# Kernel tuning notes

Measured on AMD Instinct MI355X. Metric: run time of the kernel, lower is better.

The kernel has to match this reference:

```python
import jax, jax.numpy as jnp
import numpy as np

NEG_SLOPE = 0.2


def _gat_layer(x, src, dst, W, att_src, att_dst, bias, concat):
    # x: [N, Fin], W: [Fin, H*C], att_*: [H, C], bias: [H*C] or [C]
    N = x.shape[0]
    H, C = att_src.shape
    h = (x @ W).reshape(N, H, C)                      # node features per head
    a_src = jnp.sum(h * att_src, axis=-1)             # [N, H]
    a_dst = jnp.sum(h * att_dst, axis=-1)             # [N, H]
    e = jax.nn.leaky_relu(a_src[src] + a_dst[dst], NEG_SLOPE)  # [E, H]
    # segment softmax over destination nodes
    m = jax.ops.segment_max(e, dst, num_segments=N)   # [N, H]
    m = jnp.where(jnp.isfinite(m), m, 0.0)
    ex = jnp.exp(e - m[dst])
    s = jax.ops.segment_sum(ex, dst, num_segments=N)  # [N, H]
    alpha = ex / (s[dst] + 1e-16)                     # [E, H]
    msg = h[src] * alpha[:, :, None]                  # [E, H, C]
    out = jax.ops.segment_sum(msg, dst, num_segments=N)  # [N, H, C]
    out = out.reshape(N, H * C) if concat else out.mean(axis=1)
    return out + bias


def setup_inputs() -> dict:
    key = jax.random.key(0)
    ks = jax.random.split(key, 20)
    N, E, Fin, Cg, H = 50000, 800000, 128, 64, 4
    HC = H * Cg
    s = 0.1
    x = jax.random.normal(ks[0], (N, Fin), jnp.float32)
    edge_index = jax.random.randint(ks[1], (2, E), 0, N, dtype=jnp.int32)
    inp = {
        'x': x,
        'edge_index': edge_index,
        'W0': jax.random.normal(ks[2], (Fin, HC), jnp.float32) * s,
        'as0': jax.random.normal(ks[3], (H, Cg), jnp.float32) * s,
        'ad0': jax.random.normal(ks[4], (H, Cg), jnp.float32) * s,
        'b0': jnp.zeros((HC,), jnp.float32),
        'W1': jax.random.normal(ks[5], (HC, HC), jnp.float32) * s,
        'as1': jax.random.normal(ks[6], (H, Cg), jnp.float32) * s,
        'ad1': jax.random.normal(ks[7], (H, Cg), jnp.float32) * s,
        'b1': jnp.zeros((HC,), jnp.float32),
        'W2': jax.random.normal(ks[8], (HC, HC), jnp.float32) * s,
        'as2': jax.random.normal(ks[9], (H, Cg), jnp.float32) * s,
        'ad2': jax.random.normal(ks[10], (H, Cg), jnp.float32) * s,
        'b2': jnp.zeros((Cg,), jnp.float32),
        # linear head: 64 -> 128 -> 10
        'lw0': jax.random.normal(ks[11], (Cg, 128), jnp.float32) * s,
        'lb0': jnp.zeros((128,), jnp.float32),
        'lw1': jax.random.normal(ks[12], (128, 10), jnp.float32) * s,
        'lb1': jnp.zeros((10,), jnp.float32),
    }
    return inp


def reference(x, edge_index, W0, as0, ad0, b0, W1, as1, ad1, b1,
              W2, as2, ad2, b2, lw0, lb0, lw1, lb1):
    N = x.shape[0]
    # PyG GATConv add_self_loops=True: append self-loop edges
    loop = jnp.arange(N, dtype=edge_index.dtype)
    src = jnp.concatenate([edge_index[0], loop])
    dst = jnp.concatenate([edge_index[1], loop])
    h = _gat_layer(x, src, dst, W0, as0, ad0, b0, True)
    h = _gat_layer(h, src, dst, W1, as1, ad1, b1, True)
    h = _gat_layer(h, src, dst, W2, as2, ad2, b2, False)
    h = jax.nn.relu(h @ lw0 + lb0)
    return h @ lw1 + lb1
```

## Files before the change

### kernel.cpp

```cpp
#include <hip/hip_runtime.h>
#include <hip/hip_bf16.h>

#define HEADS 4
#define CH 64
#define HC 256

typedef __attribute__((ext_vector_type(8))) short short8;
typedef __attribute__((ext_vector_type(4))) float f32x4;
typedef __attribute__((ext_vector_type(8))) _Float16 half8;

typedef __attribute__((address_space(1))) const unsigned int as1_uint;
typedef __attribute__((address_space(3))) unsigned int as3_uint;

__device__ __forceinline__ void gll16(const void* g, void* l){
  __builtin_amdgcn_global_load_lds((as1_uint*)g, (as3_uint*)l, 16, 0, 0);
}

__device__ inline unsigned short f2bf(float f){
  unsigned u = __float_as_uint(f);
  return (unsigned short)((u + 0x7FFF + ((u >> 16) & 1)) >> 16);
}


__global__ void hist_kernel(const int* __restrict__ dst, int E, int ET, int* __restrict__ cnt){
  int e = blockIdx.x * blockDim.x + threadIdx.x;
  if (e >= ET) return;
  int d = (e < E) ? dst[e] : (e - E);
  atomicAdd(&cnt[d], 1);
}

__global__ void blocksum_kernel(const int* __restrict__ cnt, int N, int* __restrict__ bsum){
  int tid = threadIdx.x;
  int i = blockIdx.x * 256 + tid;
  int v = (i < N) ? cnt[i] : 0;
  #pragma unroll
  for (int off = 32; off >= 1; off >>= 1) v += __shfl_xor(v, off);
  __shared__ int ws[4];
  if ((tid & 63) == 0) ws[tid >> 6] = v;
  __syncthreads();
  if (tid == 0) bsum[blockIdx.x] = ws[0] + ws[1] + ws[2] + ws[3];
}

__global__ void scanb_kernel(int* __restrict__ bsum, int nb){
  __shared__ int buf[256];
  int tid = threadIdx.x;
  int v = (tid < nb) ? bsum[tid] : 0;
  buf[tid] = v;
  __syncthreads();
  #pragma unroll
  for (int off = 1; off < 256; off <<= 1){
    int t = (tid >= off) ? buf[tid - off] : 0;
    __syncthreads();
    buf[tid] += t;
    __syncthreads();
  }
  if (tid < nb) bsum[tid] = buf[tid] - v;
}

__global__ void scanfinal_kernel(const int* __restrict__ cnt, const int* __restrict__ bsum,
                                 int* __restrict__ ptr, int* __restrict__ cur, int N){
  __shared__ int buf[256];
  int tid = threadIdx.x;
  int i = blockIdx.x * 256 + tid;
  int v = (i < N) ? cnt[i] : 0;
  buf[tid] = v;
  __syncthreads();
  #pragma unroll
  for (int off = 1; off < 256; off <<= 1){
    int t = (tid >= off) ? buf[tid - off] : 0;
    __syncthreads();
    buf[tid] += t;
    __syncthreads();
  }
  int exc = buf[tid] - v + bsum[blockIdx.x];
  if (i < N){
    ptr[i] = exc; cur[i] = exc;
    if (i == N - 1) ptr[N] = exc + v;
  }
}

__global__ void scatter_kernel(const int* __restrict__ src, const int* __restrict__ dst,
                               int E, int ET, int* __restrict__ cur,
                               int* __restrict__ csr_src, int* __restrict__ csr_dst){
  int e = blockIdx.x * blockDim.x + threadIdx.x;
  if (e >= ET) return;
  int s, d;
  if (e < E){ s = src[e]; d = dst[e]; } else { s = e - E; d = e - E; }
  int pos = atomicAdd(&cur[d], 1);
  csr_src[pos] = s;
  csr_dst[pos] = d;
}


__global__ void dhist_kernel(const int* __restrict__ cnt, int N, int* __restrict__ dbins){
  __shared__ int lb[64];
  int tid = threadIdx.x;
  if (tid < 64) lb[tid] = 0;
  __syncthreads();
  int n = blockIdx.x * 256 + tid;
  if (n < N) atomicAdd(&lb[min(cnt[n], 63)], 1);
  __syncthreads();
  if (tid < 64 && lb[tid]) atomicAdd(&dbins[tid], lb[tid]);
}

__global__ void dscan_kernel(int* __restrict__ dbins, int* __restrict__ dcur){
  int lane = threadIdx.x;
  int v = dbins[lane];
  int s = v;
  #pragma unroll
  for (int off = 1; off < 64; off <<= 1){
    int t = __shfl_up(s, off);
    if (lane >= off) s += t;
  }
  int exc = s - v;
  dbins[lane] = exc;
  dcur[lane] = exc;
}

__global__ void dscatter_kernel(const int* __restrict__ cnt, int N, int* __restrict__ dcur,
                                int* __restrict__ perm){
  __shared__ int lb[64];
  __shared__ int base[64];
  int tid = threadIdx.x;
  if (tid < 64) lb[tid] = 0;
  __syncthreads();
  int n = blockIdx.x * 256 + tid;
  bool valid = n < N;
  int bin = 0, rank = 0;
  if (valid){
    bin = min(cnt[n], 63);
    rank = atomicAdd(&lb[bin], 1);
  }
  __syncthreads();
  if (tid < 64) base[tid] = lb[tid] ? atomicAdd(&dcur[tid], lb[tid]) : 0;
  __syncthreads();
  if (valid) perm[base[bin] + rank] = n;
}


__global__ void ew_kernel(const int* __restrict__ csr_src, const int* __restrict__ csr_dst,
                          const float* __restrict__ a_src, const float* __restrict__ a_dst,
                          float* __restrict__ w, int ET){
  int i = blockIdx.x * 256 + threadIdx.x;
  if (i >= ET) return;
  int s = csr_src[i], d = csr_dst[i];
  float4 as = *(const float4*)&a_src[(size_t)s * 4];
  float4 ad = *(const float4*)&a_dst[(size_t)d * 4];
  float4 r;
  float e;
  e = as.x + ad.x; e = e > 0.f ? e : 0.2f * e; r.x = __expf(e);
  e = as.y + ad.y; e = e > 0.f ? e : 0.2f * e; r.y = __expf(e);
  e = as.z + ad.z; e = e > 0.f ? e : 0.2f * e; r.z = __expf(e);
  e = as.w + ad.w; e = e > 0.f ? e : 0.2f * e; r.w = __expf(e);
  *(float4*)&w[(size_t)i * 4] = r;
}


__global__ void wsplit_kernel(const float* __restrict__ W0, unsigned short* __restrict__ h0,
                              unsigned short* __restrict__ l0,
                              const float* __restrict__ W1, unsigned short* __restrict__ h1,
                              unsigned short* __restrict__ l1,
                              const float* __restrict__ W2, unsigned short* __restrict__ h2,
                              unsigned short* __restrict__ l2){
  int idx = blockIdx.x * 256 + threadIdx.x;
  const float* W; unsigned short *hi, *lo; int K;
  if (idx < 128 * HC){ W = W0; hi = h0; lo = l0; K = 128; }
  else if (idx < (128 + 256) * HC){ idx -= 128 * HC; W = W1; hi = h1; lo = l1; K = 256; }
  else { idx -= (128 + 256) * HC; W = W2; hi = h2; lo = l2; K = 256; }
  int k = idx >> 8, n = idx & 255;
  float w = W[idx];
  unsigned short hb = f2bf(w);
  float hf = __uint_as_float((unsigned)hb << 16);
  unsigned short lb = f2bf(w - hf);
  hi[(size_t)n * K + k] = hb;
  lo[(size_t)n * K + k] = lb;
}


__global__ void xsplit_kernel(const float* __restrict__ x, int total4,
                              unsigned short* __restrict__ xhi, unsigned short* __restrict__ xlo){
  int i4 = blockIdx.x * 256 + threadIdx.x;
  if (i4 >= total4) return;
  float4 v = *(const float4*)&x[(size_t)i4 * 4];
  float va[4] = {v.x, v.y, v.z, v.w};
  unsigned short h4[4], l4[4];
  #pragma unroll
  for (int j = 0; j < 4; j++){
    unsigned short hb = f2bf(va[j]);
    float hf = __uint_as_float((unsigned)hb << 16);
    h4[j] = hb;
    l4[j] = f2bf(va[j] - hf);
  }
  *(ushort4*)&xhi[(size_t)i4 * 4] = make_ushort4(h4[0], h4[1], h4[2], h4[3]);
  *(ushort4*)&xlo[(size_t)i4 * 4] = make_ushort4(l4[0], l4[1], l4[2], l4[3]);
}


__global__ void lwsplit_kernel(const float* __restrict__ lw0,
                               unsigned short* __restrict__ l0hi, unsigned short* __restrict__ l0lo,
                               const float* __restrict__ lw1, _Float16* __restrict__ l1T){
  int idx = blockIdx.x * 256 + threadIdx.x;
  if (idx < 8192){
    int n = idx & 127, k = idx >> 7;
    float w = lw0[k * 128 + n];
    unsigned short hb = f2bf(w);
    float hf = __uint_as_float((unsigned)hb << 16);
    unsigned short lb = f2bf(w - hf);
    l0hi[n * 64 + k] = hb;
    l0lo[n * 64 + k] = lb;
  } else if (idx < 8192 + 2048){
    int id = idx - 8192;
    int n = id & 15, k = id >> 4;
    float w = (n < 10) ? lw1[k * 10 + n] : 0.f;
    l1T[n * 128 + k] = (_Float16)w;
  }
}


__launch_bounds__(256, 2)
__global__ void gemm_mfma_kernel(const unsigned short* __restrict__ Ahi,
                                 const unsigned short* __restrict__ Alo,
                                 const unsigned short* __restrict__ BhiT,
                                 const unsigned short* __restrict__ BloT,
                                 _Float16* __restrict__ Cm,
                                 const float* __restrict__ att_s, const float* __restrict__ att_d,
                                 float* __restrict__ a_src, float* __restrict__ a_dst,
                                 int K){
  __shared__ __align__(16) unsigned short L[2][4][4096];

  int tid = threadIdx.x;
  int m0 = blockIdx.x * 128, n0 = blockIdx.y * 128;
  int wave = tid >> 6, lane = tid & 63;
  int wm = (wave >> 1) * 64, wn = (wave & 1) * 64;
  int col = lane & 15, quad = lane >> 4;

  f32x4 acc[4][4];
  #pragma unroll
  for (int a = 0; a < 4; a++)
    #pragma unroll
    for (int b = 0; b < 4; b++)
      acc[a][b] = (f32x4){0.f, 0.f, 0.f, 0.f};

  const int nIter = K >> 5;

  auto stage = [&](int buf, int kk){
    #pragma unroll
    for (int i = 0; i < 2; i++){
      int slotbase = (wave * 2 + i) * 64;
      int slot = slotbase + lane;
      int m = slot >> 2;
      int q = (lane & 3) ^ ((m >> 1) & 3);
      size_t ga = (size_t)(m0 + m) * K + kk + q * 8;
      size_t gb = (size_t)(n0 + m) * K + kk + q * 8;
      int lo = slotbase * 8;
      gll16(&Ahi[ga],  &L[buf][0][lo]);
      gll16(&Alo[ga],  &L[buf][1][lo]);
      gll16(&BhiT[gb], &L[buf][2][lo]);
      gll16(&BloT[gb], &L[buf][3][lo]);
    }
  };

  stage(0, 0);

  for (int it = 0; it < nIter; it++){
    int buf = it & 1;
    __syncthreads();
    if (it + 1 < nIter) stage(buf ^ 1, (it + 1) << 5);

    short8 af[4][2], bf[4][2];
    #pragma unroll
    for (int t = 0; t < 4; t++){
      int rmA = wm + t * 16 + col;
      int rmB = wn + t * 16 + col;
      int sA = rmA * 4 + (quad ^ ((rmA >> 1) & 3));
      int sB = rmB * 4 + (quad ^ ((rmB >> 1) & 3));
      af[t][0] = *(const short8*)&L[buf][0][sA * 8];
      af[t][1] = *(const short8*)&L[buf][1][sA * 8];
      bf[t][0] = *(const short8*)&L[buf][2][sB * 8];
      bf[t][1] = *(const short8*)&L[buf][3][sB * 8];
    }
    #pragma unroll
    for (int mt = 0; mt < 4; mt++)
      #pragma unroll
      for (int nt = 0; nt < 4; nt++){
        acc[mt][nt] = __builtin_amdgcn_mfma_f32_16x16x32_bf16(af[mt][0], bf[nt][0], acc[mt][nt], 0, 0, 0);
        acc[mt][nt] = __builtin_amdgcn_mfma_f32_16x16x32_bf16(af[mt][1], bf[nt][0], acc[mt][nt], 0, 0, 0);
        acc[mt][nt] = __builtin_amdgcn_mfma_f32_16x16x32_bf16(af[mt][0], bf[nt][1], acc[mt][nt], 0, 0, 0);
      }
  }

  #pragma unroll
  for (int mt = 0; mt < 4; mt++)
    #pragma unroll
    for (int nt = 0; nt < 4; nt++){
      int colg = n0 + wn + nt * 16 + col;
      #pragma unroll
      for (int r = 0; r < 4; r++){
        int row = m0 + wm + mt * 16 + quad * 4 + r;
        Cm[(size_t)row * HC + colg] = (_Float16)acc[mt][nt][r];
      }
    }

  int head = (n0 + wn) >> 6;
  float asv[4], adv[4];
  #pragma unroll
  for (int nt = 0; nt < 4; nt++){
    asv[nt] = att_s[head * CH + nt * 16 + col];
    adv[nt] = att_d[head * CH + nt * 16 + col];
  }
  #pragma unroll
  for (int mt = 0; mt < 4; mt++){
    float sp[4] = {0.f,0.f,0.f,0.f}, dp[4] = {0.f,0.f,0.f,0.f};
    #pragma unroll
    for (int nt = 0; nt < 4; nt++)
      #pragma unroll
      for (int r = 0; r < 4; r++){
        sp[r] += acc[mt][nt][r] * asv[nt];
        dp[r] += acc[mt][nt][r] * adv[nt];
      }
    #pragma unroll
    for (int off = 1; off <= 8; off <<= 1)
      #pragma unroll
      for (int r = 0; r < 4; r++){
        sp[r] += __shfl_xor(sp[r], off);
        dp[r] += __shfl_xor(dp[r], off);
      }
    if (col == 0){
      #pragma unroll
      for (int r = 0; r < 4; r++){
        int row = m0 + wm + mt * 16 + quad * 4 + r;
        a_src[row * HEADS + head] = sp[r];
        a_dst[row * HEADS + head] = dp[r];
      }
    }
  }
}


__global__ void agg_kernel(const _Float16* __restrict__ h, const float* __restrict__ w,
                           const int* __restrict__ ptr, const int* __restrict__ csr_src,
                           const int* __restrict__ perm,
                           const float* __restrict__ bias,
                           unsigned short* __restrict__ out_hi, unsigned short* __restrict__ out_lo,
                           int mean_mode, const float* __restrict__ b2,
                           float* __restrict__ f2){
  __shared__ float sm[HEADS][8][CH];
  int head = threadIdx.x >> 6;
  int lane = threadIdx.x & 63;
  int slot = lane >> 3, c8 = lane & 7;
  int pn = perm[blockIdx.x * 8 + slot];
  int beg = 0, deg = 0;
  if (pn >= 0){ beg = ptr[pn]; deg = ptr[pn + 1] - beg; }

  int maxdeg = deg;
  #pragma unroll
  for (int off = 8; off <= 32; off <<= 1) maxdeg = max(maxdeg, __shfl_xor(maxdeg, off));

  float acc[8] = {0.f,0.f,0.f,0.f,0.f,0.f,0.f,0.f};
  float ss = 0.f;
  int it = 0;
  for (; it + 4 <= maxdeg; it += 4){
    int idx[4]; float wv[4];
    #pragma unroll
    for (int k = 0; k < 4; k++)
      idx[k] = beg + ((it + k < deg) ? it + k : 0);
    int s0 = csr_src[idx[0]], s1 = csr_src[idx[1]];
    int s2 = csr_src[idx[2]], s3 = csr_src[idx[3]];
    #pragma unroll
    for (int k = 0; k < 4; k++)
      wv[k] = (it + k < deg) ? w[(size_t)idx[k] * 4 + head] : 0.f;
    half8 h0 = *(const half8*)&h[(size_t)s0 * HC + head * CH + c8 * 8];
    half8 h1 = *(const half8*)&h[(size_t)s1 * HC + head * CH + c8 * 8];
    half8 h2 = *(const half8*)&h[(size_t)s2 * HC + head * CH + c8 * 8];
    half8 h3 = *(const half8*)&h[(size_t)s3 * HC + head * CH + c8 * 8];
    #pragma unroll
    for (int j = 0; j < 8; j++){
      acc[j] += wv[0] * (float)h0[j];
      acc[j] += wv[1] * (float)h1[j];
      acc[j] += wv[2] * (float)h2[j];
      acc[j] += wv[3] * (float)h3[j];
    }
    ss += wv[0] + wv[1] + wv[2] + wv[3];
  }
  for (; it < maxdeg; ++it){
    bool valid = it < deg;
    int idx = beg + (valid ? it : 0);
    int s = csr_src[idx];
    float wv = valid ? w[(size_t)idx * 4 + head] : 0.f;
    half8 hv = *(const half8*)&h[(size_t)s * HC + head * CH + c8 * 8];
    #pragma unroll
    for (int j = 0; j < 8; j++) acc[j] += wv * (float)hv[j];
    ss += wv;
  }
  float inv = 1.f / (ss + 1e-16f);
  #pragma unroll
  for (int j = 0; j < 8; j++) acc[j] *= inv;

  if (!mean_mode){
    if (pn >= 0){
      const float* bp = &bias[head * CH + c8 * 8];
      short8 hi8, lo8;
      #pragma unroll
      for (int j = 0; j < 8; j++){
        float v = acc[j] + bp[j];
        unsigned short hb = f2bf(v);
        float hf = __uint_as_float((unsigned)hb << 16);
        hi8[j] = (short)hb;
        lo8[j] = (short)f2bf(v - hf);
      }
      size_t o = (size_t)pn * HC + head * CH + c8 * 8;
      *(short8*)&out_hi[o] = hi8;
      *(short8*)&out_lo[o] = lo8;
    }
  } else {
    #pragma unroll
    for (int j = 0; j < 8; j++) sm[head][slot][c8 * 8 + j] = acc[j];
    __syncthreads();
    for (int t = threadIdx.x; t < 512; t += 256){
      int sl = t >> 6, ch = t & 63;
      int pn2 = perm[blockIdx.x * 8 + sl];
      if (pn2 >= 0)
        f2[(size_t)pn2 * CH + ch] =
          0.25f * (sm[0][sl][ch] + sm[1][sl][ch] + sm[2][sl][ch] + sm[3][sl][ch]) + b2[ch];
    }
  }
}


__launch_bounds__(256, 2)
__global__ void head_mfma_kernel(const float* __restrict__ f2,
                                 const unsigned short* __restrict__ lw0hiT,
                                 const unsigned short* __restrict__ lw0loT,
                                 const _Float16* __restrict__ lw1T,
                                 const float* __restrict__ lb0,
                                 const float* __restrict__ lb1,
                                 float* __restrict__ outp, int N){
  __shared__ __align__(16) unsigned short L[27648];
  __shared__ __align__(16) _Float16 Ls[16][136];
  const int tid = threadIdx.x;
  const int wave = tid >> 6, lane = tid & 63;
  const int col = lane & 15, quad = lane >> 4;
  const int m0 = blockIdx.x * 64;

  { int n = tid >> 4, k = (tid & 15) * 8;
    *(half8*)&Ls[n][k] = *(const half8*)&lw1T[n * 128 + k]; }

  #pragma unroll
  for (int r = 0; r < 2; r++){
    int id = r * 256 + tid;
    int m = id >> 3, q = id & 7;
    int gm = m0 + m;
    float va[8];
    if (gm < N){
      float4 v0 = *(const float4*)&f2[(size_t)gm * CH + q * 8];
      float4 v1 = *(const float4*)&f2[(size_t)gm * CH + q * 8 + 4];
      va[0]=v0.x; va[1]=v0.y; va[2]=v0.z; va[3]=v0.w;
      va[4]=v1.x; va[5]=v1.y; va[6]=v1.z; va[7]=v1.w;
    } else {
      #pragma unroll
      for (int j = 0; j < 8; j++) va[j] = 0.f;
    }
    short8 hi8, lo8;
    #pragma unroll
    for (int j = 0; j < 8; j++){
      unsigned short hb = f2bf(va[j]);
      float hf = __uint_as_float((unsigned)hb << 16);
      hi8[j] = (short)hb;
      lo8[j] = (short)f2bf(va[j] - hf);
    }
    *(short8*)&L[m * 72 + q * 8] = hi8;
    *(short8*)&L[4608 + m * 72 + q * 8] = lo8;
  }
  #pragma unroll
  for (int r = 0; r < 4; r++){
    int id = r * 256 + tid;
    int n = id >> 3, q = id & 7;
    *(short8*)&L[9216 + n * 72 + q * 8]  = *(const short8*)&lw0hiT[n * 64 + q * 8];
    *(short8*)&L[18432 + n * 72 + q * 8] = *(const short8*)&lw0loT[n * 64 + q * 8];
  }
  __syncthreads();

  const int wn = wave * 32;
  f32x4 acc[4][2];
  #pragma unroll
  for (int a = 0; a < 4; a++)
    #pragma unroll
    for (int b = 0; b < 2; b++) acc[a][b] = (f32x4){0.f,0.f,0.f,0.f};

  #pragma unroll
  for (int ks = 0; ks < 2; ks++){
    int k = ks * 32 + quad * 8;
    short8 ah[4], al[4], bh[2], bl[2];
    #pragma unroll
    for (int mt = 0; mt < 4; mt++){
      ah[mt] = *(short8*)&L[(mt * 16 + col) * 72 + k];
      al[mt] = *(short8*)&L[4608 + (mt * 16 + col) * 72 + k];
    }
    #pragma unroll
    for (int nt = 0; nt < 2; nt++){
      bh[nt] = *(short8*)&L[9216 + (wn + nt * 16 + col) * 72 + k];
      bl[nt] = *(short8*)&L[18432 + (wn + nt * 16 + col) * 72 + k];
    }
    #pragma unroll
    for (int mt = 0; mt < 4; mt++)
      #pragma unroll
      for (int nt = 0; nt < 2; nt++){
        acc[mt][nt] = __builtin_amdgcn_mfma_f32_16x16x32_bf16(ah[mt], bh[nt], acc[mt][nt], 0, 0, 0);
        acc[mt][nt] = __builtin_amdgcn_mfma_f32_16x16x32_bf16(al[mt], bh[nt], acc[mt][nt], 0, 0, 0);
        acc[mt][nt] = __builtin_amdgcn_mfma_f32_16x16x32_bf16(ah[mt], bl[nt], acc[mt][nt], 0, 0, 0);
      }
  }
  __syncthreads();

  _Float16* Zp = (_Float16*)L;
  #pragma unroll
  for (int nt = 0; nt < 2; nt++){
    int n = wn + nt * 16 + col;
    float b = lb0[n];
    #pragma unroll
    for (int mt = 0; mt < 4; mt++)
      #pragma unroll
      for (int r2 = 0; r2 < 4; r2++){
        int m = mt * 16 + quad * 4 + r2;
        float z = acc[mt][nt][r2] + b;
        Zp[m * 136 + n] = (_Float16)fmaxf(z, 0.f);
      }
  }
  __syncthreads();

  f32x4 acc2 = (f32x4){0.f,0.f,0.f,0.f};
  #pragma unroll
  for (int ks = 0; ks < 4; ks++){
    int k = ks * 32 + quad * 8;
    half8 a2 = *(half8*)&Zp[(wave * 16 + col) * 136 + k];
    half8 b2v = *(half8*)&Ls[col][k];
    acc2 = __builtin_amdgcn_mfma_f32_16x16x32_f16(a2, b2v, acc2, 0, 0, 0);
  }
  if (col < 10){
    float bb = lb1[col];
    #pragma unroll
    for (int r2 = 0; r2 < 4; r2++){
      int row = m0 + wave * 16 + quad * 4 + r2;
      if (row < N) outp[(size_t)row * 10 + col] = acc2[r2] + bb;
    }
  }
}


extern "C" void kernel_launch(void* const* d_in, const int* in_sizes, int n_in,
                              void* d_out, int out_size, void* d_ws, size_t ws_size,
                              hipStream_t stream) {
  const float* x   = (const float*)d_in[0];
  const int*   ei  = (const int*)d_in[1];
  const float* W0  = (const float*)d_in[2];
  const float* as0 = (const float*)d_in[3];
  const float* ad0 = (const float*)d_in[4];
  const float* b0  = (const float*)d_in[5];
  const float* W1  = (const float*)d_in[6];
  const float* as1 = (const float*)d_in[7];
  const float* ad1 = (const float*)d_in[8];
  const float* b1  = (const float*)d_in[9];
  const float* W2  = (const float*)d_in[10];
  const float* as2 = (const float*)d_in[11];
  const float* ad2 = (const float*)d_in[12];
  const float* b2  = (const float*)d_in[13];
  const float* lw0 = (const float*)d_in[14];
  const float* lb0 = (const float*)d_in[15];
  const float* lw1 = (const float*)d_in[16];
  const float* lb1 = (const float*)d_in[17];
  float* outp = (float*)d_out;

  int N  = in_sizes[0] / 128;
  int E  = in_sizes[1] / 2;
  int ET = E + N;
  int nb = (N + 255) / 256;
  int Mp = ((N + 127) / 128) * 128;
  int Np8 = ((N + 7) / 8) * 8;

  char* ws = (char*)d_ws;
  _Float16* Hb = (_Float16*)ws;       ws += (size_t)Mp * HC * sizeof(_Float16);
  unsigned short* Fhi = (unsigned short*)ws; ws += (size_t)Mp * HC * 2;
  unsigned short* Flo = (unsigned short*)ws; ws += (size_t)Mp * HC * 2;
  float* f2  = (float*)ws; ws += (size_t)N * CH * sizeof(float);
  float* a_s = (float*)ws; ws += (size_t)Mp * HEADS * sizeof(float);
  float* a_d = (float*)ws; ws += (size_t)Mp * HEADS * sizeof(float);
  float* ewt = (float*)ws; ws += (size_t)ET * HEADS * sizeof(float);
  int* cnt   = (int*)ws;   ws += (size_t)N * sizeof(int);
  int* cur   = (int*)ws;   ws += (size_t)N * sizeof(int);
  int* ptrA  = (int*)ws;   ws += (size_t)(N + 1) * sizeof(int);
  int* bsum  = (int*)ws;   ws += (size_t)nb * sizeof(int);
  int* csr   = (int*)ws;   ws += (size_t)ET * sizeof(int);
  int* csrd  = (int*)ws;   ws += (size_t)ET * sizeof(int);
  int* perm  = (int*)ws;   ws += (size_t)Np8 * sizeof(int);
  int* dbins = (int*)ws;   ws += 64 * sizeof(int);
  int* dcur  = (int*)ws;   ws += 64 * sizeof(int);
  unsigned short* w0hi = (unsigned short*)ws; ws += (size_t)128 * HC * 2;
  unsigned short* w0lo = (unsigned short*)ws; ws += (size_t)128 * HC * 2;
  unsigned short* w1hi = (unsigned short*)ws; ws += (size_t)HC * HC * 2;
  unsigned short* w1lo = (unsigned short*)ws; ws += (size_t)HC * HC * 2;
  unsigned short* w2hi = (unsigned short*)ws; ws += (size_t)HC * HC * 2;
  unsigned short* w2lo = (unsigned short*)ws; ws += (size_t)HC * HC * 2;
  unsigned short* l0hi = (unsigned short*)ws; ws += (size_t)8192 * 2;
  unsigned short* l0lo = (unsigned short*)ws; ws += (size_t)8192 * 2;
  _Float16* l1T        = (_Float16*)ws;       ws += (size_t)2048 * 2;

  const int* srcArr = ei;
  const int* dstArr = ei + E;

  hipMemsetAsync(cnt, 0, (size_t)N * sizeof(int), stream);
  hipMemsetAsync(dbins, 0, 64 * sizeof(int), stream);
  hipMemsetAsync(perm, 0xFF, (size_t)Np8 * sizeof(int), stream);
  hist_kernel<<<(ET + 255) / 256, 256, 0, stream>>>(dstArr, E, ET, cnt);
  blocksum_kernel<<<nb, 256, 0, stream>>>(cnt, N, bsum);
  scanb_kernel<<<1, 256, 0, stream>>>(bsum, nb);
  scanfinal_kernel<<<nb, 256, 0, stream>>>(cnt, bsum, ptrA, cur, N);
  scatter_kernel<<<(ET + 255) / 256, 256, 0, stream>>>(srcArr, dstArr, E, ET, cur, csr, csrd);

  dhist_kernel<<<nb, 256, 0, stream>>>(cnt, N, dbins);
  dscan_kernel<<<1, 64, 0, stream>>>(dbins, dcur);
  dscatter_kernel<<<nb, 256, 0, stream>>>(cnt, N, dcur, perm);

  wsplit_kernel<<<((128 + 256 + 256) * HC) / 256, 256, 0, stream>>>(
      W0, w0hi, w0lo, W1, w1hi, w1lo, W2, w2hi, w2lo);
  lwsplit_kernel<<<(8192 + 2048 + 255) / 256, 256, 0, stream>>>(lw0, l0hi, l0lo, lw1, l1T);
  xsplit_kernel<<<(N * 128 / 4 + 255) / 256, 256, 0, stream>>>(x, N * 128 / 4, Fhi, Flo);

  dim3 ggrid(Mp / 128, 2);
  int eb = (ET + 255) / 256;
  int ab = Np8 / 8;

  gemm_mfma_kernel<<<ggrid, 256, 0, stream>>>(Fhi, Flo, w0hi, w0lo, Hb, as0, ad0, a_s, a_d, 128);
  ew_kernel<<<eb, 256, 0, stream>>>(csr, csrd, a_s, a_d, ewt, ET);
  agg_kernel<<<ab, 256, 0, stream>>>(Hb, ewt, ptrA, csr, perm, b0, Fhi, Flo, 0, nullptr, nullptr);

  gemm_mfma_kernel<<<ggrid, 256, 0, stream>>>(Fhi, Flo, w1hi, w1lo, Hb, as1, ad1, a_s, a_d, HC);
  ew_kernel<<<eb, 256, 0, stream>>>(csr, csrd, a_s, a_d, ewt, ET);
  agg_kernel<<<ab, 256, 0, stream>>>(Hb, ewt, ptrA, csr, perm, b1, Fhi, Flo, 0, nullptr, nullptr);

  gemm_mfma_kernel<<<ggrid, 256, 0, stream>>>(Fhi, Flo, w2hi, w2lo, Hb, as2, ad2, a_s, a_d, HC);
  ew_kernel<<<eb, 256, 0, stream>>>(csr, csrd, a_s, a_d, ewt, ET);
  agg_kernel<<<ab, 256, 0, stream>>>(Hb, ewt, ptrA, csr, perm, nullptr, nullptr, nullptr, 1, b2, f2);

  head_mfma_kernel<<<(N + 63) / 64, 256, 0, stream>>>(f2, l0hi, l0lo, l1T, lb0, lb1, outp, N);
}
```

Measured before the change: 561.5 us.

## Fuse edge-weight computation into aggregation and stage GEMM output through LDS

Removes the separate per-edge weight kernel and its ET x 4 float buffer. The aggregation kernel now gathers a_src per source, reads a_dst once per destination, and computes the leaky-relu and exp inline. The scatter no longer writes csr_dst. The GEMM epilogue writes its fp16 output tile to shared memory first and then stores full coalesced 16-byte rows, instead of scattered 2-byte stores. The cost is more exp work per edge inside agg (once per c8 lane) and an extra small gather of a_src.

```diff
diff --git a/kernel.cpp b/kernel.cpp
--- a/kernel.cpp
+++ b/kernel.cpp
@@ -81,14 +81,13 @@
 
 __global__ void scatter_kernel(const int* __restrict__ src, const int* __restrict__ dst,
                                int E, int ET, int* __restrict__ cur,
-                               int* __restrict__ csr_src, int* __restrict__ csr_dst){
+                               int* __restrict__ csr_src){
   int e = blockIdx.x * blockDim.x + threadIdx.x;
   if (e >= ET) return;
   int s, d;
   if (e < E){ s = src[e]; d = dst[e]; } else { s = e - E; d = e - E; }
   int pos = atomicAdd(&cur[d], 1);
   csr_src[pos] = s;
-  csr_dst[pos] = d;
 }
 
 
@@ -135,24 +134,6 @@
   if (tid < 64) base[tid] = lb[tid] ? atomicAdd(&dcur[tid], lb[tid]) : 0;
   __syncthreads();
   if (valid) perm[base[bin] + rank] = n;
-}
-
-
-__global__ void ew_kernel(const int* __restrict__ csr_src, const int* __restrict__ csr_dst,
-                          const float* __restrict__ a_src, const float* __restrict__ a_dst,
-                          float* __restrict__ w, int ET){
-  int i = blockIdx.x * 256 + threadIdx.x;
-  if (i >= ET) return;
-  int s = csr_src[i], d = csr_dst[i];
-  float4 as = *(const float4*)&a_src[(size_t)s * 4];
-  float4 ad = *(const float4*)&a_dst[(size_t)d * 4];
-  float4 r;
-  float e;
-  e = as.x + ad.x; e = e > 0.f ? e : 0.2f * e; r.x = __expf(e);
-  e = as.y + ad.y; e = e > 0.f ? e : 0.2f * e; r.y = __expf(e);
-  e = as.z + ad.z; e = e > 0.f ? e : 0.2f * e; r.z = __expf(e);
-  e = as.w + ad.w; e = e > 0.f ? e : 0.2f * e; r.w = __expf(e);
-  *(float4*)&w[(size_t)i * 4] = r;
 }
 
 
@@ -289,18 +270,6 @@
       }
   }
 
-  #pragma unroll
-  for (int mt = 0; mt < 4; mt++)
-    #pragma unroll
-    for (int nt = 0; nt < 4; nt++){
-      int colg = n0 + wn + nt * 16 + col;
-      #pragma unroll
-      for (int r = 0; r < 4; r++){
-        int row = m0 + wm + mt * 16 + quad * 4 + r;
-        Cm[(size_t)row * HC + colg] = (_Float16)acc[mt][nt][r];
-      }
-    }
-
   int head = (n0 + wn) >> 6;
   float asv[4], adv[4];
   #pragma unroll
@@ -334,10 +303,34 @@
       }
     }
   }
-}
-
-
-__global__ void agg_kernel(const _Float16* __restrict__ h, const float* __restrict__ w,
+
+  __syncthreads();
+  _Float16* Cs = (_Float16*)&L[0][0][0];
+  #pragma unroll
+  for (int mt = 0; mt < 4; mt++)
+    #pragma unroll
+    for (int nt = 0; nt < 4; nt++){
+      int cl = wn + nt * 16 + col;
+      #pragma unroll
+      for (int r = 0; r < 4; r++){
+        int rl = wm + mt * 16 + quad * 4 + r;
+        Cs[rl * 136 + cl] = (_Float16)acc[mt][nt][r];
+      }
+    }
+  __syncthreads();
+  {
+    int row = tid >> 1, half = tid & 1;
+    size_t gbase = (size_t)(m0 + row) * HC + n0 + half * 64;
+    const _Float16* srcp = &Cs[row * 136 + half * 64];
+    #pragma unroll
+    for (int j = 0; j < 8; j++)
+      *(half8*)&Cm[gbase + j * 8] = *(const half8*)&srcp[j * 8];
+  }
+}
+
+
+__global__ void agg_kernel(const _Float16* __restrict__ h,
+                           const float* __restrict__ a_src, const float* __restrict__ a_dst,
                            const int* __restrict__ ptr, const int* __restrict__ csr_src,
                            const int* __restrict__ perm,
                            const float* __restrict__ bias,
@@ -350,7 +343,8 @@
   int slot = lane >> 3, c8 = lane & 7;
   int pn = perm[blockIdx.x * 8 + slot];
   int beg = 0, deg = 0;
-  if (pn >= 0){ beg = ptr[pn]; deg = ptr[pn + 1] - beg; }
+  float adst = 0.f;
+  if (pn >= 0){ beg = ptr[pn]; deg = ptr[pn + 1] - beg; adst = a_dst[pn * HEADS + head]; }
 
   int maxdeg = deg;
   #pragma unroll
@@ -360,19 +354,25 @@
   float ss = 0.f;
   int it = 0;
   for (; it + 4 <= maxdeg; it += 4){
-    int idx[4]; float wv[4];
-    #pragma unroll
-    for (int k = 0; k < 4; k++)
-      idx[k] = beg + ((it + k < deg) ? it + k : 0);
-    int s0 = csr_src[idx[0]], s1 = csr_src[idx[1]];
-    int s2 = csr_src[idx[2]], s3 = csr_src[idx[3]];
-    #pragma unroll
-    for (int k = 0; k < 4; k++)
-      wv[k] = (it + k < deg) ? w[(size_t)idx[k] * 4 + head] : 0.f;
-    half8 h0 = *(const half8*)&h[(size_t)s0 * HC + head * CH + c8 * 8];
-    half8 h1 = *(const half8*)&h[(size_t)s1 * HC + head * CH + c8 * 8];
-    half8 h2 = *(const half8*)&h[(size_t)s2 * HC + head * CH + c8 * 8];
-    half8 h3 = *(const half8*)&h[(size_t)s3 * HC + head * CH + c8 * 8];
+    int s[4]; float as4[4];
+    #pragma unroll
+    for (int k = 0; k < 4; k++){
+      int idx = beg + ((it + k < deg) ? it + k : 0);
+      s[k] = csr_src[idx];
+    }
+    #pragma unroll
+    for (int k = 0; k < 4; k++) as4[k] = a_src[s[k] * HEADS + head];
+    half8 h0 = *(const half8*)&h[(size_t)s[0] * HC + head * CH + c8 * 8];
+    half8 h1 = *(const half8*)&h[(size_t)s[1] * HC + head * CH + c8 * 8];
+    half8 h2 = *(const half8*)&h[(size_t)s[2] * HC + head * CH + c8 * 8];
+    half8 h3 = *(const half8*)&h[(size_t)s[3] * HC + head * CH + c8 * 8];
+    float wv[4];
+    #pragma unroll
+    for (int k = 0; k < 4; k++){
+      float e = as4[k] + adst;
+      e = e > 0.f ? e : 0.2f * e;
+      wv[k] = (it + k < deg) ? __expf(e) : 0.f;
+    }
     #pragma unroll
     for (int j = 0; j < 8; j++){
       acc[j] += wv[0] * (float)h0[j];
@@ -386,7 +386,9 @@
     bool valid = it < deg;
     int idx = beg + (valid ? it : 0);
     int s = csr_src[idx];
-    float wv = valid ? w[(size_t)idx * 4 + head] : 0.f;
+    float e = a_src[s * HEADS + head] + adst;
+    e = e > 0.f ? e : 0.2f * e;
+    float wv = valid ? __expf(e) : 0.f;
     half8 hv = *(const half8*)&h[(size_t)s * HC + head * CH + c8 * 8];
     #pragma unroll
     for (int j = 0; j < 8; j++) acc[j] += wv * (float)hv[j];
@@ -584,13 +586,11 @@
   float* f2  = (float*)ws; ws += (size_t)N * CH * sizeof(float);
   float* a_s = (float*)ws; ws += (size_t)Mp * HEADS * sizeof(float);
   float* a_d = (float*)ws; ws += (size_t)Mp * HEADS * sizeof(float);
-  float* ewt = (float*)ws; ws += (size_t)ET * HEADS * sizeof(float);
   int* cnt   = (int*)ws;   ws += (size_t)N * sizeof(int);
   int* cur   = (int*)ws;   ws += (size_t)N * sizeof(int);
   int* ptrA  = (int*)ws;   ws += (size_t)(N + 1) * sizeof(int);
   int* bsum  = (int*)ws;   ws += (size_t)nb * sizeof(int);
   int* csr   = (int*)ws;   ws += (size_t)ET * sizeof(int);
-  int* csrd  = (int*)ws;   ws += (size_t)ET * sizeof(int);
   int* perm  = (int*)ws;   ws += (size_t)Np8 * sizeof(int);
   int* dbins = (int*)ws;   ws += 64 * sizeof(int);
   int* dcur  = (int*)ws;   ws += 64 * sizeof(int);
@@ -614,7 +614,7 @@
   blocksum_kernel<<<nb, 256, 0, stream>>>(cnt, N, bsum);
   scanb_kernel<<<1, 256, 0, stream>>>(bsum, nb);
   scanfinal_kernel<<<nb, 256, 0, stream>>>(cnt, bsum, ptrA, cur, N);
-  scatter_kernel<<<(ET + 255) / 256, 256, 0, stream>>>(srcArr, dstArr, E, ET, cur, csr, csrd);
+  scatter_kernel<<<(ET + 255) / 256, 256, 0, stream>>>(srcArr, dstArr, E, ET, cur, csr);
 
   dhist_kernel<<<nb, 256, 0, stream>>>(cnt, N, dbins);
   dscan_kernel<<<1, 64, 0, stream>>>(dbins, dcur);
@@ -626,20 +626,16 @@
   xsplit_kernel<<<(N * 128 / 4 + 255) / 256, 256, 0, stream>>>(x, N * 128 / 4, Fhi, Flo);
 
   dim3 ggrid(Mp / 128, 2);
-  int eb = (ET + 255) / 256;
   int ab = Np8 / 8;
 
   gemm_mfma_kernel<<<ggrid, 256, 0, stream>>>(Fhi, Flo, w0hi, w0lo, Hb, as0, ad0, a_s, a_d, 128);
-  ew_kernel<<<eb, 256, 0, stream>>>(csr, csrd, a_s, a_d, ewt, ET);
-  agg_kernel<<<ab, 256, 0, stream>>>(Hb, ewt, ptrA, csr, perm, b0, Fhi, Flo, 0, nullptr, nullptr);
+  agg_kernel<<<ab, 256, 0, stream>>>(Hb, a_s, a_d, ptrA, csr, perm, b0, Fhi, Flo, 0, nullptr, nullptr);
 
   gemm_mfma_kernel<<<ggrid, 256, 0, stream>>>(Fhi, Flo, w1hi, w1lo, Hb, as1, ad1, a_s, a_d, HC);
-  ew_kernel<<<eb, 256, 0, stream>>>(csr, csrd, a_s, a_d, ewt, ET);
-  agg_kernel<<<ab, 256, 0, stream>>>(Hb, ewt, ptrA, csr, perm, b1, Fhi, Flo, 0, nullptr, nullptr);
+  agg_kernel<<<ab, 256, 0, stream>>>(Hb, a_s, a_d, ptrA, csr, perm, b1, Fhi, Flo, 0, nullptr, nullptr);
 
   gemm_mfma_kernel<<<ggrid, 256, 0, stream>>>(Fhi, Flo, w2hi, w2lo, Hb, as2, ad2, a_s, a_d, HC);
-  ew_kernel<<<eb, 256, 0, stream>>>(csr, csrd, a_s, a_d, ewt, ET);
-  agg_kernel<<<ab, 256, 0, stream>>>(Hb, ewt, ptrA, csr, perm, nullptr, nullptr, nullptr, 1, b2, f2);
+  agg_kernel<<<ab, 256, 0, stream>>>(Hb, a_s, a_d, ptrA, csr, perm, nullptr, nullptr, nullptr, 1, b2, f2);
 
   head_mfma_kernel<<<(N + 63) / 64, 256, 0, stream>>>(f2, l0hi, l0lo, l1T, lb0, lb1, outp, N);
 }
```

After: 570.2 us. Within noise of the previous version (+1.5%).
